# Kernel optimization log

Hardware: AMD Instinct MI355X
Metric: run time of the kernel (lower is better)

Reference implementation:

```python
import jax, jax.numpy as jnp
import numpy as np

B, K, F, INCH, OUTCH, R = 16, 8, 512, 512, 512, 8


def setup_inputs() -> dict:
    key = jax.random.key(0)
    ks = jax.random.split(key, 10)
    inp = {
        "x": jax.random.normal(ks[0], (B, K, F, INCH), jnp.float32),
        "u": jax.random.normal(ks[1], (B, K, OUTCH, R), jnp.float32),
        "v": jax.random.normal(ks[2], (B, K, INCH, R), jnp.float32),
        "b": jax.random.normal(ks[3], (B, 1, 1, OUTCH), jnp.float32) * 0.02,
        # learned parameters (torch nn.Linear layout: W [out, in])
        "W_pass": jax.random.normal(ks[4], (INCH // 2, INCH), jnp.float32) * 0.02,
        "b_pass": jax.random.normal(ks[5], (INCH // 2,), jnp.float32) * 0.02,
        "W_ave": jax.random.normal(ks[6], (INCH // 2, INCH), jnp.float32) * 0.02,
        "b_ave": jax.random.normal(ks[7], (INCH // 2,), jnp.float32) * 0.02,
        "W_out": jax.random.normal(ks[8], (OUTCH, INCH), jnp.float32) * 0.02,
        "b_out": jax.random.normal(ks[9], (OUTCH,), jnp.float32) * 0.02,
    }
    return inp


def reference(x, u, v, b, W_pass, b_pass, W_ave, b_ave, W_out, b_out):
    # x: [B,K,F,inch]
    k = x.shape[1]
    # 'ave' branch: linear -> mean over K -> broadcast back to K
    y = jnp.einsum('bkfi,hi->bkfh', x, W_ave) + b_ave        # [B,K,F,inch//2]
    y = jnp.broadcast_to(jnp.mean(y, axis=1, keepdims=True), y.shape)
    # 'pass' branch
    xp = jnp.einsum('bkfi,hi->bkfh', x, W_pass) + b_pass      # [B,K,F,inch//2]
    h = jnp.concatenate([xp, y], axis=-1)                     # [B,K,F,inch]
    h = jax.nn.gelu(h, approximate=False)                     # dropout is identity in eval
    # LoRA term: mean(v * h) over inch, then mean(u * z) over R
    inch = h.shape[-1]
    r = v.shape[-1]
    z = jnp.einsum('bkfi,bkir->bkfr', h, v) / inch            # [B,K,F,R]
    lora = jnp.einsum('bkfr,bkor->bkfo', z, u) / r            # [B,K,F,outch]
    out = jnp.einsum('bkfi,oi->bkfo', h, W_out) + b_out + lora + b
    out = jax.nn.gelu(out, approximate=False)
    return out
```

## Files before the change

kernel.cpp:

```cpp
#include <hip/hip_runtime.h>
#include <stdint.h>


typedef __attribute__((ext_vector_type(8))) __bf16 bf16x8;
typedef __attribute__((ext_vector_type(4))) float f32x4;
typedef __attribute__((ext_vector_type(8))) unsigned short ushort8;
typedef __attribute__((ext_vector_type(4))) unsigned short ushort4_t;
typedef __attribute__((ext_vector_type(4))) float float4_t;

#define MFMA16(a, b, c) __builtin_amdgcn_mfma_f32_16x16x32_bf16((a), (b), (c), 0, 0, 0)
#define GLL16(g, l)                                                                   \
    __builtin_amdgcn_global_load_lds((const __attribute__((address_space(1))) void*)(g), \
                                     (__attribute__((address_space(3))) void*)(l), 16, 0, 0)

__device__ inline unsigned short f2bf(float f) {
    union { float fv; unsigned u; } un; un.fv = f;
    unsigned u = un.u;
    u += 0x7FFFu + ((u >> 16) & 1u);
    return (unsigned short)(u >> 16);
}

__device__ inline float geluf(float x) {
    float x2 = x * x;
    float inner = x + 0.044715f * x * x2;
    float e = __expf(-1.5957691216057308f * inner);
    return x * __builtin_amdgcn_rcpf(1.0f + e);
}

__device__ inline bf16x8 lds8(const unsigned short* p) {
    return __builtin_bit_cast(bf16x8, *(const ushort8*)p);
}

__device__ inline void stage_chunk(const unsigned short* __restrict__ src, long rowbase,
                                   long stride, int k0, unsigned short* buf, int c, int l) {
    const int r = c * 16 + (l >> 2);
    const int j = (l & 3) ^ ((l >> 2) & 3) ^ (l >> 4);
    GLL16(src + (rowbase + r) * stride + k0 + j * 8, &buf[c * 512]);
}

__device__ inline bf16x8 ldf2(const unsigned short* buf, int rbase, int l) {
    const int r = rbase + (l & 15);
    const int slot = (l >> 4) ^ (r & 3) ^ ((r >> 2) & 3);
    return lds8(&buf[r * 32 + slot * 8]);
}

__device__ inline void stage_w(const unsigned short* __restrict__ src, long rowbase,
                               long stride, int k0, unsigned short* buf, int l) {
#pragma unroll
    for (int it = 0; it < 4; ++it) {
        const int s = it * 64 + l;
        const int r = s >> 2;
        const int j = (s & 3) ^ (r & 3);
        GLL16(src + (rowbase + r) * stride + k0 + j * 8, &buf[it * 512]);
    }
}

__device__ inline bf16x8 ldw(const unsigned short* buf, int rbase, int l) {
    const int r = rbase + (l & 15);
    const int j = l >> 4;
    return lds8(&buf[r * 32 + (((j ^ r) & 3) << 3)]);
}

__global__ void cvt_all(const float* __restrict__ a, const float* __restrict__ b,
                        const float* __restrict__ c, unsigned short* __restrict__ oa,
                        unsigned short* __restrict__ ob, unsigned short* __restrict__ oc) {
    int bid = blockIdx.x;
    const float* s; unsigned short* d; int off;
    if (bid < 128) { s = a; d = oa; off = bid; }
    else if (bid < 256) { s = b; d = ob; off = bid - 128; }
    else { s = c; d = oc; off = bid - 256; }
    int i = off * 256 + threadIdx.x;
    float4_t v = *(const float4_t*)(s + (size_t)i * 4);
    ushort4_t r;
    r[0] = f2bf(v[0]); r[1] = f2bf(v[1]); r[2] = f2bf(v[2]); r[3] = f2bf(v[3]);
    *(ushort4_t*)(d + (size_t)i * 4) = r;
}

__global__ void mean_cvt(const float* __restrict__ x,
                         unsigned short* __restrict__ xb,
                         unsigned short* __restrict__ xm) {
    int gid = blockIdx.x * 256 + threadIdx.x;
    int c  = gid & 63;
    int bf = gid >> 6;
    int b  = bf >> 9;
    int f  = bf & 511;
    float s0 = 0.f, s1 = 0.f, s2 = 0.f, s3 = 0.f, s4 = 0.f, s5 = 0.f, s6 = 0.f, s7 = 0.f;
#pragma unroll
    for (int k = 0; k < 8; ++k) {
        long row = (long)(b * 8 + k) * 512 + f;
        float4_t lo = *(const float4_t*)(x + row * 512 + c * 8);
        float4_t hi = *(const float4_t*)(x + row * 512 + c * 8 + 4);
        s0 += lo[0]; s1 += lo[1]; s2 += lo[2]; s3 += lo[3];
        s4 += hi[0]; s5 += hi[1]; s6 += hi[2]; s7 += hi[3];
        ushort8 t;
        t[0] = f2bf(lo[0]); t[1] = f2bf(lo[1]); t[2] = f2bf(lo[2]); t[3] = f2bf(lo[3]);
        t[4] = f2bf(hi[0]); t[5] = f2bf(hi[1]); t[6] = f2bf(hi[2]); t[7] = f2bf(hi[3]);
        *(ushort8*)(xb + row * 512 + c * 8) = t;
    }
    ushort8 m;
    m[0] = f2bf(s0 * 0.125f); m[1] = f2bf(s1 * 0.125f);
    m[2] = f2bf(s2 * 0.125f); m[3] = f2bf(s3 * 0.125f);
    m[4] = f2bf(s4 * 0.125f); m[5] = f2bf(s5 * 0.125f);
    m[6] = f2bf(s6 * 0.125f); m[7] = f2bf(s7 * 0.125f);
    *(ushort8*)(xm + (long)bf * 512 + c * 8) = m;
}

__launch_bounds__(256)
__global__ void gemm_gelu(const unsigned short* __restrict__ A,
                          const unsigned short* __restrict__ W,
                          const float* __restrict__ bias,
                          unsigned short* __restrict__ O,
                          int chunk) {
    __shared__ __align__(16) unsigned short S[32768];
    const int tid = threadIdx.x;
    const int w = tid >> 6, l = tid & 63;
    const int wr = w >> 1, wc = w & 1;
    const int work = ((blockIdx.x & 7) * chunk) + (blockIdx.x >> 3);
    const int nt = work & 1;
    const int mt = work >> 1;
    const long row0 = (long)mt * 128 + wr * 64;
    const long col0 = (long)nt * 128 + wc * 64;

    unsigned short* aw[2] = { &S[w * 4096],        &S[16384 + w * 4096] };
    unsigned short* bw[2] = { &S[w * 4096 + 2048], &S[16384 + w * 4096 + 2048] };

    f32x4 acc[4][4];
    const f32x4 z4 = {0.f, 0.f, 0.f, 0.f};
#pragma unroll
    for (int i = 0; i < 4; ++i)
#pragma unroll
        for (int j = 0; j < 4; ++j) acc[i][j] = z4;

    stage_w(A, row0, 512, 0, aw[0], l);
    stage_w(W, col0, 512, 0, bw[0], l);

#pragma unroll
    for (int t = 0; t < 16; ++t) {
        if (t < 15) {
            stage_w(A, row0, 512, (t + 1) * 32, aw[(t + 1) & 1], l);
            stage_w(W, col0, 512, (t + 1) * 32, bw[(t + 1) & 1], l);
            asm volatile("s_waitcnt vmcnt(8)" ::: "memory");
        } else {
            asm volatile("s_waitcnt vmcnt(0)" ::: "memory");
        }
        const unsigned short* ab = aw[t & 1];
        const unsigned short* bbuf = bw[t & 1];
        bf16x8 af[4], bfr[4];
#pragma unroll
        for (int mi = 0; mi < 4; ++mi) af[mi] = ldw(ab, mi * 16, l);
#pragma unroll
        for (int nj = 0; nj < 4; ++nj) bfr[nj] = ldw(bbuf, nj * 16, l);
        __builtin_amdgcn_s_setprio(1);
#pragma unroll
        for (int mi = 0; mi < 4; ++mi)
#pragma unroll
            for (int nj = 0; nj < 4; ++nj)
                acc[mi][nj] = MFMA16(af[mi], bfr[nj], acc[mi][nj]);
        __builtin_amdgcn_s_setprio(0);
    }

    __syncthreads();
    const int colblk = nt * 128;
#pragma unroll
    for (int mi = 0; mi < 4; ++mi) {
        const int R0 = wr * 64 + mi * 16 + (l >> 4) * 4;
#pragma unroll
        for (int nj = 0; nj < 4; ++nj) {
            const int C = wc * 64 + nj * 16 + (l & 15);
            const float bv = bias[colblk + C];
#pragma unroll
            for (int q = 0; q < 4; ++q)
                S[(R0 + q) * 136 + C] = f2bf(geluf(acc[mi][nj][q] + bv));
        }
    }
    __syncthreads();
    const long rowt = (long)mt * 128;
#pragma unroll
    for (int s = 0; s < 8; ++s) {
        const int flat = s * 2048 + tid * 8;
        const int row = flat >> 7;
        const int col = flat & 127;
        ushort8 vv = *(const ushort8*)&S[row * 136 + col];
        *(ushort8*)(O + (rowt + row) * 256 + colblk + col) = vv;
    }
}

__launch_bounds__(256)
__global__ void g2calc(const unsigned short* __restrict__ Gy,
                       const unsigned short* __restrict__ Wo,
                       const float* __restrict__ bo,
                       float* __restrict__ G2) {
    __shared__ __align__(16) unsigned short S[32768];
    const int tid = threadIdx.x;
    const int w = tid >> 6, l = tid & 63;
    const int wr = w >> 1, wc = w & 1;
    const int mt = blockIdx.x >> 2;
    const int nt = blockIdx.x & 3;
    const long row0 = (long)mt * 128 + wr * 64;
    const long col0 = (long)nt * 128 + wc * 64;

    unsigned short* aw[2] = { &S[w * 4096],        &S[16384 + w * 4096] };
    unsigned short* bw[2] = { &S[w * 4096 + 2048], &S[16384 + w * 4096 + 2048] };

    f32x4 acc[4][4];
    const f32x4 z4 = {0.f, 0.f, 0.f, 0.f};
#pragma unroll
    for (int i = 0; i < 4; ++i)
#pragma unroll
        for (int j = 0; j < 4; ++j) acc[i][j] = z4;

    stage_w(Gy, row0, 256, 0, aw[0], l);
    stage_w(Wo, col0, 512, 256, bw[0], l);

#pragma unroll
    for (int t = 0; t < 8; ++t) {
        if (t < 7) {
            stage_w(Gy, row0, 256, (t + 1) * 32, aw[(t + 1) & 1], l);
            stage_w(Wo, col0, 512, 256 + (t + 1) * 32, bw[(t + 1) & 1], l);
            asm volatile("s_waitcnt vmcnt(8)" ::: "memory");
        } else {
            asm volatile("s_waitcnt vmcnt(0)" ::: "memory");
        }
        const unsigned short* ab = aw[t & 1];
        const unsigned short* bbuf = bw[t & 1];
        bf16x8 af[4], bfr[4];
#pragma unroll
        for (int mi = 0; mi < 4; ++mi) af[mi] = ldw(ab, mi * 16, l);
#pragma unroll
        for (int nj = 0; nj < 4; ++nj) bfr[nj] = ldw(bbuf, nj * 16, l);
#pragma unroll
        for (int mi = 0; mi < 4; ++mi)
#pragma unroll
            for (int nj = 0; nj < 4; ++nj)
                acc[mi][nj] = MFMA16(af[mi], bfr[nj], acc[mi][nj]);
    }

#pragma unroll
    for (int mi = 0; mi < 4; ++mi) {
        const long rb = row0 + mi * 16 + (l >> 4) * 4;
#pragma unroll
        for (int nj = 0; nj < 4; ++nj) {
            const long cg = col0 + nj * 16 + (l & 15);
            const float bv = bo[cg];
#pragma unroll
            for (int q = 0; q < 4; ++q)
                G2[(rb + q) * 512 + cg] = acc[mi][nj][q] + bv;
        }
    }
}

__launch_bounds__(512)
__global__ void fused_out(const unsigned short* __restrict__ xb,
                          const unsigned short* __restrict__ Wp,
                          const float* __restrict__ bp,
                          const unsigned short* __restrict__ Gy,
                          const unsigned short* __restrict__ Wo,
                          const float* __restrict__ bbi,
                          const float* __restrict__ u,
                          const float* __restrict__ v,
                          const float* __restrict__ G2,
                          float* __restrict__ Out) {
    __shared__ __align__(16) unsigned short hp_t[128 * 256];
    __shared__ __align__(16) unsigned short stg[2 * 12288];
    __shared__ __align__(16) unsigned short Vt[16 * 536];
    __shared__ __align__(16) unsigned short Zs[128 * 32];

    const int tid = threadIdx.x;
    const int w = tid >> 6, l = tid & 63;
    const int wm = w >> 2, wn = w & 3;
    const int mt = ((blockIdx.x & 7) * 64) + (blockIdx.x >> 3);
    const long row0 = (long)mt * 128;
    const int bk = mt >> 2;
    const int bi = bk >> 3;
    const int f0 = (mt & 3) * 128;
    const long gyb = (long)bi * 512 + f0;

    const f32x4 zero4 = {0.f, 0.f, 0.f, 0.f};

    {
        f32x4 acc[4][4];
#pragma unroll
        for (int i = 0; i < 4; ++i)
#pragma unroll
            for (int j = 0; j < 4; ++j) acc[i][j] = zero4;

#define STAGE1(t)                                                             \
    {                                                                         \
        const int kb = (t) * 32;                                              \
        unsigned short* bA = &stg[((t) & 1) * 12288];                         \
        unsigned short* bB = bA + 4096;                                       \
        stage_chunk(xb, row0, 512, kb, bA, w, l);                             \
        stage_chunk(Wp, 0, 512, kb, bB, 2 * w, l);                            \
        stage_chunk(Wp, 0, 512, kb, bB, 2 * w + 1, l);                        \
    }

        STAGE1(0)
#pragma unroll
        for (int t = 0; t < 16; ++t) {
            __builtin_amdgcn_s_barrier();
            if (t < 15) {
                STAGE1(t + 1)
                asm volatile("s_waitcnt vmcnt(3)" ::: "memory");
            } else {
                asm volatile("s_waitcnt vmcnt(0)" ::: "memory");
            }
            const unsigned short* bA = &stg[(t & 1) * 12288];
            const unsigned short* bB = bA + 4096;
            bf16x8 a[4], b[4];
#pragma unroll
            for (int mi = 0; mi < 4; ++mi) a[mi] = ldf2(bA, wm * 64 + mi * 16, l);
#pragma unroll
            for (int nj = 0; nj < 4; ++nj) b[nj] = ldf2(bB, wn * 64 + nj * 16, l);
            __builtin_amdgcn_s_setprio(1);
#pragma unroll
            for (int mi = 0; mi < 4; ++mi)
#pragma unroll
                for (int nj = 0; nj < 4; ++nj)
                    acc[mi][nj] = MFMA16(a[mi], b[nj], acc[mi][nj]);
            __builtin_amdgcn_s_setprio(0);
        }
#undef STAGE1

#pragma unroll
        for (int mi = 0; mi < 4; ++mi) {
            const int R0 = wm * 64 + mi * 16 + (l >> 4) * 4;
#pragma unroll
            for (int nj = 0; nj < 4; ++nj) {
                const int C = wn * 64 + nj * 16 + (l & 15);
                const float bv = bp[C];
#pragma unroll
                for (int q = 0; q < 4; ++q) {
                    const int row = R0 + q;
                    const int slot = (C >> 3) ^ (row & 31);
                    hp_t[row * 256 + slot * 8 + (C & 7)] =
                        f2bf(geluf(acc[mi][nj][q] + bv));
                }
            }
        }
        ushort8 zz = {0, 0, 0, 0, 0, 0, 0, 0};
        *(ushort8*)&Zs[tid * 8] = zz;
        for (int i = tid; i < 1072; i += 512) *(ushort8*)&Vt[i * 8] = zz;
    }
    __syncthreads();

#define STAGE2(t)                                                              \
    {                                                                          \
        const int ch = (t) >> 3;                                               \
        const int kb = ((t) & 7) * 32;                                         \
        unsigned short* bB = &stg[((t) & 1) * 12288];                          \
        stage_chunk(Wo, (long)ch * 256, 512, kb, bB, 2 * w, l);                \
        stage_chunk(Wo, (long)ch * 256, 512, kb, bB, 2 * w + 1, l);            \
    }
    STAGE2(0)
    {
        const float* vp = v + (long)bk * 4096;
        float4_t v0 = *(const float4_t*)(vp + tid * 8);
        float4_t v1 = *(const float4_t*)(vp + tid * 8 + 4);
#pragma unroll
        for (int j = 0; j < 8; ++j) {
            const int flat = tid * 8 + j;
            const float val = (j < 4 ? v0[j] : v1[j - 4]) * (1.0f / 512.0f);
            Vt[(flat & 7) * 536 + (flat >> 3)] = f2bf(val);
        }
    }
    __syncthreads();

    {
        f32x4 zacc = zero4;
        const int zrow = w * 16 + (l & 15);
#pragma unroll
        for (int ks = 0; ks < 8; ++ks) {
            const int jw = ks * 4 + (l >> 4);
            bf16x8 av = lds8(&hp_t[zrow * 256 + ((jw ^ (zrow & 31)) * 8)]);
            bf16x8 bv = lds8(&Vt[(l & 15) * 536 + ks * 32 + (l >> 4) * 8]);
            zacc = MFMA16(av, bv, zacc);
        }
        const unsigned short* grow = Gy + (gyb + zrow) * 256 + (l >> 4) * 8;
#pragma unroll
        for (int ks = 0; ks < 8; ++ks) {
            bf16x8 bv = lds8(&Vt[(l & 15) * 536 + 256 + ks * 32 + (l >> 4) * 8]);
            zacc = MFMA16(lds8(grow + ks * 32), bv, zacc);
        }
        if ((l & 15) < 8) {
#pragma unroll
            for (int reg = 0; reg < 4; ++reg)
                Zs[(w * 16 + (l >> 4) * 4 + reg) * 32 + (l & 15)] = f2bf(zacc[reg]);
        }
    }

    f32x4 acc2[2][4][4];
#pragma unroll
    for (int c = 0; c < 2; ++c)
#pragma unroll
        for (int i = 0; i < 4; ++i)
#pragma unroll
            for (int j = 0; j < 4; ++j) acc2[c][i][j] = zero4;

#pragma unroll
    for (int t = 0; t < 16; ++t) {
        __builtin_amdgcn_s_barrier();
        if (t < 15) {
            STAGE2(t + 1)
            asm volatile("s_waitcnt vmcnt(2)" ::: "memory");
        } else {
            asm volatile("s_waitcnt vmcnt(0)" ::: "memory");
        }
        const unsigned short* bB = &stg[(t & 1) * 12288];
        bf16x8 a[4], b[4];
#pragma unroll
        for (int mi = 0; mi < 4; ++mi) {
            const int row = wm * 64 + mi * 16 + (l & 15);
            const int jw = (t & 7) * 4 + (l >> 4);
            a[mi] = lds8(&hp_t[row * 256 + ((jw ^ (row & 31)) * 8)]);
        }
#pragma unroll
        for (int nj = 0; nj < 4; ++nj) b[nj] = ldf2(bB, wn * 64 + nj * 16, l);
        __builtin_amdgcn_s_setprio(1);
#pragma unroll
        for (int mi = 0; mi < 4; ++mi)
#pragma unroll
            for (int nj = 0; nj < 4; ++nj)
                acc2[t >> 3][mi][nj] = MFMA16(a[mi], b[nj], acc2[t >> 3][mi][nj]);
        __builtin_amdgcn_s_setprio(0);
    }
#undef STAGE2

    const float* up = u + (long)bk * 4096;
#pragma unroll
    for (int ch = 0; ch < 2; ++ch) {
#pragma unroll
        for (int nj = 0; nj < 4; ++nj) {
            const int og = ch * 256 + wn * 64 + nj * 16 + (l & 15);
            ushort8 ubits = {0, 0, 0, 0, 0, 0, 0, 0};
            if ((l >> 4) == 0) {
                float4_t u0 = *(const float4_t*)(up + og * 8);
                float4_t u1 = *(const float4_t*)(up + og * 8 + 4);
                ubits[0] = f2bf(u0[0] * 0.125f); ubits[1] = f2bf(u0[1] * 0.125f);
                ubits[2] = f2bf(u0[2] * 0.125f); ubits[3] = f2bf(u0[3] * 0.125f);
                ubits[4] = f2bf(u1[0] * 0.125f); ubits[5] = f2bf(u1[1] * 0.125f);
                ubits[6] = f2bf(u1[2] * 0.125f); ubits[7] = f2bf(u1[3] * 0.125f);
            }
            bf16x8 ub = __builtin_bit_cast(bf16x8, ubits);
#pragma unroll
            for (int mi = 0; mi < 4; ++mi) {
                bf16x8 az = lds8(&Zs[(wm * 64 + mi * 16 + (l & 15)) * 32 + (l >> 4) * 8]);
                acc2[ch][mi][nj] = MFMA16(az, ub, acc2[ch][mi][nj]);
            }
        }
    }

#pragma unroll
    for (int ch = 0; ch < 2; ++ch) {
#pragma unroll
        for (int nj = 0; nj < 4; ++nj) {
            const int og = ch * 256 + wn * 64 + nj * 16 + (l & 15);
            const float badd = bbi[bi * 512 + og];
#pragma unroll
            for (int mi = 0; mi < 4; ++mi) {
                const int R0 = wm * 64 + mi * 16 + (l >> 4) * 4;
#pragma unroll
                for (int q = 0; q < 4; ++q) {
                    const float g2v = G2[(gyb + R0 + q) * 512 + og];
                    __builtin_nontemporal_store(
                        geluf(acc2[ch][mi][nj][q] + badd + g2v),
                        Out + (row0 + R0 + q) * 512 + og);
                }
            }
        }
    }
}

extern "C" void kernel_launch(void* const* d_in, const int* in_sizes, int n_in,
                              void* d_out, int out_size, void* d_ws, size_t ws_size,
                              hipStream_t stream) {
    const float* x  = (const float*)d_in[0];
    const float* u  = (const float*)d_in[1];
    const float* v  = (const float*)d_in[2];
    const float* bb = (const float*)d_in[3];
    const float* Wp = (const float*)d_in[4];
    const float* bp = (const float*)d_in[5];
    const float* Wa = (const float*)d_in[6];
    const float* ba = (const float*)d_in[7];
    const float* Wo = (const float*)d_in[8];
    const float* bo = (const float*)d_in[9];
    float* out = (float*)d_out;

    char* ws = (char*)d_ws;
    unsigned short* xb  = (unsigned short*)(ws + 0);
    unsigned short* xm  = (unsigned short*)(ws + 67108864);
    unsigned short* gy  = (unsigned short*)(ws + 75497472);
    float*          G2  = (float*)(ws + 79691776);
    unsigned short* Wpb = (unsigned short*)(ws + 96468992);
    unsigned short* Wab = (unsigned short*)(ws + 96731136);
    unsigned short* Wob = (unsigned short*)(ws + 96993280);

    cvt_all<<<512, 256, 0, stream>>>(Wp, Wa, Wo, Wpb, Wab, Wob);
    mean_cvt<<<2048, 256, 0, stream>>>(x, xb, xm);
    gemm_gelu<<<128, 256, 0, stream>>>(xm, Wab, ba, gy, 16);
    g2calc<<<256, 256, 0, stream>>>(gy, Wob, bo, G2);
    fused_out<<<512, 512, 0, stream>>>(xb, Wpb, bp, gy, Wob, bb, u, v, G2, out);
}
```

Before: 148.1 us.

## Halve fused_out row tile to 64 and restructure pipelines for higher occupancy

The fused output kernel now processes 64-row tiles instead of 128, with 1024 blocks, smaller LDS buffers and accumulator arrays, and launch bounds asking for 4 blocks per CU. The pass-GEMM is split into two 128-column chunks written to hp_t at chunk ends, the output GEMM runs over four 128-column chunks, and the LoRA MFMA is merged into the epilogue. The goal is to cut register and LDS pressure so more waves hide latency. The cost is that each block reloads the full weight matrices for half as many rows, so weight traffic per output row doubles, and the loops add extra barriers.

Result: slower. 154.9 us (+4.6%).

```diff
diff --git a/kernel.cpp b/kernel.cpp
--- a/kernel.cpp
+++ b/kernel.cpp
@@ -249,7 +249,7 @@
     }
 }
 
-__launch_bounds__(512)
+__launch_bounds__(512, 4)
 __global__ void fused_out(const unsigned short* __restrict__ xb,
                           const unsigned short* __restrict__ Wp,
                           const float* __restrict__ bp,
@@ -260,99 +260,98 @@
                           const float* __restrict__ v,
                           const float* __restrict__ G2,
                           float* __restrict__ Out) {
-    __shared__ __align__(16) unsigned short hp_t[128 * 256];
-    __shared__ __align__(16) unsigned short stg[2 * 12288];
-    __shared__ __align__(16) unsigned short Vt[16 * 536];
-    __shared__ __align__(16) unsigned short Zs[128 * 32];
+    __shared__ __align__(16) unsigned short hp_t[64 * 256];
+    __shared__ __align__(16) unsigned short stg[2 * 6144];
+    __shared__ __align__(16) unsigned short Vt[16 * 520];
+    __shared__ __align__(16) unsigned short Zs[64 * 32];
 
     const int tid = threadIdx.x;
     const int w = tid >> 6, l = tid & 63;
     const int wm = w >> 2, wn = w & 3;
-    const int mt = ((blockIdx.x & 7) * 64) + (blockIdx.x >> 3);
-    const long row0 = (long)mt * 128;
-    const int bk = mt >> 2;
+    const int mt = ((blockIdx.x & 7) * 128) + (blockIdx.x >> 3);
+    const long row0 = (long)mt * 64;
+    const int bk = mt >> 3;
     const int bi = bk >> 3;
-    const int f0 = (mt & 3) * 128;
-    const long gyb = (long)bi * 512 + f0;
+    const long gyb = (long)bi * 512 + (mt & 7) * 64;
 
     const f32x4 zero4 = {0.f, 0.f, 0.f, 0.f};
 
     {
-        f32x4 acc[4][4];
-#pragma unroll
-        for (int i = 0; i < 4; ++i)
-#pragma unroll
-            for (int j = 0; j < 4; ++j) acc[i][j] = zero4;
-
-#define STAGE1(t)                                                             \
+        f32x4 acc[2][2];
+#pragma unroll
+        for (int i = 0; i < 2; ++i)
+#pragma unroll
+            for (int j = 0; j < 2; ++j) acc[i][j] = zero4;
+
+#define STG1(s)                                                               \
     {                                                                         \
-        const int kb = (t) * 32;                                              \
-        unsigned short* bA = &stg[((t) & 1) * 12288];                         \
-        unsigned short* bB = bA + 4096;                                       \
-        stage_chunk(xb, row0, 512, kb, bA, w, l);                             \
-        stage_chunk(Wp, 0, 512, kb, bB, 2 * w, l);                            \
-        stage_chunk(Wp, 0, 512, kb, bB, 2 * w + 1, l);                        \
-    }
-
-        STAGE1(0)
-#pragma unroll
-        for (int t = 0; t < 16; ++t) {
-            __builtin_amdgcn_s_barrier();
-            if (t < 15) {
-                STAGE1(t + 1)
-                asm volatile("s_waitcnt vmcnt(3)" ::: "memory");
+        const int ch_ = (s) >> 4, kb_ = ((s) & 15) * 32;                      \
+        unsigned short* base_ = &stg[((s) & 1) * 6144];                       \
+        stage_chunk(Wp, (long)ch_ * 128, 512, kb_, base_ + 2048, w, l);       \
+        if (w < 4) stage_chunk(xb, row0, 512, kb_, base_, w, l);              \
+    }
+
+        STG1(0)
+#pragma unroll
+        for (int s = 0; s < 32; ++s) {
+            if (s < 31) {
+                STG1(s + 1)
+                if (w < 4) asm volatile("s_waitcnt vmcnt(2)" ::: "memory");
+                else       asm volatile("s_waitcnt vmcnt(1)" ::: "memory");
             } else {
                 asm volatile("s_waitcnt vmcnt(0)" ::: "memory");
             }
-            const unsigned short* bA = &stg[(t & 1) * 12288];
-            const unsigned short* bB = bA + 4096;
-            bf16x8 a[4], b[4];
-#pragma unroll
-            for (int mi = 0; mi < 4; ++mi) a[mi] = ldf2(bA, wm * 64 + mi * 16, l);
-#pragma unroll
-            for (int nj = 0; nj < 4; ++nj) b[nj] = ldf2(bB, wn * 64 + nj * 16, l);
+            __builtin_amdgcn_s_barrier();
+            const unsigned short* bufA = &stg[(s & 1) * 6144];
+            const unsigned short* bufB = bufA + 2048;
+            bf16x8 a[2], b[2];
+#pragma unroll
+            for (int mi = 0; mi < 2; ++mi) a[mi] = ldf2(bufA, wm * 32 + mi * 16, l);
+#pragma unroll
+            for (int nj = 0; nj < 2; ++nj) b[nj] = ldf2(bufB, wn * 32 + nj * 16, l);
             __builtin_amdgcn_s_setprio(1);
 #pragma unroll
-            for (int mi = 0; mi < 4; ++mi)
-#pragma unroll
-                for (int nj = 0; nj < 4; ++nj)
+            for (int mi = 0; mi < 2; ++mi)
+#pragma unroll
+                for (int nj = 0; nj < 2; ++nj)
                     acc[mi][nj] = MFMA16(a[mi], b[nj], acc[mi][nj]);
             __builtin_amdgcn_s_setprio(0);
-        }
-#undef STAGE1
-
-#pragma unroll
-        for (int mi = 0; mi < 4; ++mi) {
-            const int R0 = wm * 64 + mi * 16 + (l >> 4) * 4;
-#pragma unroll
-            for (int nj = 0; nj < 4; ++nj) {
-                const int C = wn * 64 + nj * 16 + (l & 15);
-                const float bv = bp[C];
-#pragma unroll
-                for (int q = 0; q < 4; ++q) {
-                    const int row = R0 + q;
-                    const int slot = (C >> 3) ^ (row & 31);
-                    hp_t[row * 256 + slot * 8 + (C & 7)] =
-                        f2bf(geluf(acc[mi][nj][q] + bv));
+            if (s == 15 || s == 31) {
+                const int ch = s >> 4;
+#pragma unroll
+                for (int mi = 0; mi < 2; ++mi) {
+#pragma unroll
+                    for (int nj = 0; nj < 2; ++nj) {
+                        const int C = ch * 128 + wn * 32 + nj * 16 + (l & 15);
+                        const float bv = bp[C];
+#pragma unroll
+                        for (int q = 0; q < 4; ++q) {
+                            const int row = wm * 32 + mi * 16 + (l >> 4) * 4 + q;
+                            const int slot = (C >> 3) ^ (row & 31);
+                            hp_t[row * 256 + slot * 8 + (C & 7)] =
+                                f2bf(geluf(acc[mi][nj][q] + bv));
+                        }
+                        acc[mi][nj] = zero4;
+                    }
                 }
+                asm volatile("s_waitcnt lgkmcnt(0)" ::: "memory");
             }
-        }
+            __builtin_amdgcn_s_barrier();
+        }
+#undef STG1
+    }
+
+#define STG2(s)                                                               \
+    {                                                                         \
+        const int ch_ = (s) >> 3, kb_ = ((s) & 7) * 32;                       \
+        stage_chunk(Wo, (long)ch_ * 128, 512, kb_, &stg[((s) & 1) * 6144], w, l); \
+    }
+    {
+        ushort4_t z4s = {0, 0, 0, 0};
+        *(ushort4_t*)&Zs[tid * 4] = z4s;
         ushort8 zz = {0, 0, 0, 0, 0, 0, 0, 0};
-        *(ushort8*)&Zs[tid * 8] = zz;
-        for (int i = tid; i < 1072; i += 512) *(ushort8*)&Vt[i * 8] = zz;
-    }
-    __syncthreads();
-
-#define STAGE2(t)                                                              \
-    {                                                                          \
-        const int ch = (t) >> 3;                                               \
-        const int kb = ((t) & 7) * 32;                                         \
-        unsigned short* bB = &stg[((t) & 1) * 12288];                          \
-        stage_chunk(Wo, (long)ch * 256, 512, kb, bB, 2 * w, l);                \
-        stage_chunk(Wo, (long)ch * 256, 512, kb, bB, 2 * w + 1, l);            \
-    }
-    STAGE2(0)
-    {
+        for (int i = tid; i < 520; i += 512)
+            *(ushort8*)&Vt[4160 + i * 8] = zz;
         const float* vp = v + (long)bk * 4096;
         float4_t v0 = *(const float4_t*)(vp + tid * 8);
         float4_t v1 = *(const float4_t*)(vp + tid * 8 + 4);
@@ -360,25 +359,27 @@
         for (int j = 0; j < 8; ++j) {
             const int flat = tid * 8 + j;
             const float val = (j < 4 ? v0[j] : v1[j - 4]) * (1.0f / 512.0f);
-            Vt[(flat & 7) * 536 + (flat >> 3)] = f2bf(val);
-        }
-    }
-    __syncthreads();
-
-    {
+            Vt[(flat & 7) * 520 + (flat >> 3)] = f2bf(val);
+        }
+        STG2(0)
+        asm volatile("s_waitcnt lgkmcnt(0)" ::: "memory");
+        __builtin_amdgcn_s_barrier();
+    }
+
+    if (w < 4) {
         f32x4 zacc = zero4;
         const int zrow = w * 16 + (l & 15);
 #pragma unroll
         for (int ks = 0; ks < 8; ++ks) {
             const int jw = ks * 4 + (l >> 4);
             bf16x8 av = lds8(&hp_t[zrow * 256 + ((jw ^ (zrow & 31)) * 8)]);
-            bf16x8 bv = lds8(&Vt[(l & 15) * 536 + ks * 32 + (l >> 4) * 8]);
+            bf16x8 bv = lds8(&Vt[(l & 15) * 520 + ks * 32 + (l >> 4) * 8]);
             zacc = MFMA16(av, bv, zacc);
         }
         const unsigned short* grow = Gy + (gyb + zrow) * 256 + (l >> 4) * 8;
 #pragma unroll
         for (int ks = 0; ks < 8; ++ks) {
-            bf16x8 bv = lds8(&Vt[(l & 15) * 536 + 256 + ks * 32 + (l >> 4) * 8]);
+            bf16x8 bv = lds8(&Vt[(l & 15) * 520 + 256 + ks * 32 + (l >> 4) * 8]);
             zacc = MFMA16(lds8(grow + ks * 32), bv, zacc);
         }
         if ((l & 15) < 8) {
@@ -386,51 +387,53 @@
             for (int reg = 0; reg < 4; ++reg)
                 Zs[(w * 16 + (l >> 4) * 4 + reg) * 32 + (l & 15)] = f2bf(zacc[reg]);
         }
-    }
-
-    f32x4 acc2[2][4][4];
-#pragma unroll
-    for (int c = 0; c < 2; ++c)
-#pragma unroll
-        for (int i = 0; i < 4; ++i)
-#pragma unroll
-            for (int j = 0; j < 4; ++j) acc2[c][i][j] = zero4;
-
-#pragma unroll
-    for (int t = 0; t < 16; ++t) {
-        __builtin_amdgcn_s_barrier();
-        if (t < 15) {
-            STAGE2(t + 1)
-            asm volatile("s_waitcnt vmcnt(2)" ::: "memory");
+        asm volatile("s_waitcnt lgkmcnt(0)" ::: "memory");
+    }
+
+    f32x4 acc2[4][2][2];
+#pragma unroll
+    for (int c = 0; c < 4; ++c)
+#pragma unroll
+        for (int i = 0; i < 2; ++i)
+#pragma unroll
+            for (int j = 0; j < 2; ++j) acc2[c][i][j] = zero4;
+
+#pragma unroll
+    for (int s = 0; s < 32; ++s) {
+        if (s < 31) {
+            STG2(s + 1)
+            asm volatile("s_waitcnt vmcnt(1)" ::: "memory");
         } else {
             asm volatile("s_waitcnt vmcnt(0)" ::: "memory");
         }
-        const unsigned short* bB = &stg[(t & 1) * 12288];
-        bf16x8 a[4], b[4];
-#pragma unroll
-        for (int mi = 0; mi < 4; ++mi) {
-            const int row = wm * 64 + mi * 16 + (l & 15);
-            const int jw = (t & 7) * 4 + (l >> 4);
+        __builtin_amdgcn_s_barrier();
+        const unsigned short* bufB = &stg[(s & 1) * 6144];
+        bf16x8 a[2], b[2];
+#pragma unroll
+        for (int mi = 0; mi < 2; ++mi) {
+            const int row = wm * 32 + mi * 16 + (l & 15);
+            const int jw = (s & 7) * 4 + (l >> 4);
             a[mi] = lds8(&hp_t[row * 256 + ((jw ^ (row & 31)) * 8)]);
         }
 #pragma unroll
-        for (int nj = 0; nj < 4; ++nj) b[nj] = ldf2(bB, wn * 64 + nj * 16, l);
+        for (int nj = 0; nj < 2; ++nj) b[nj] = ldf2(bufB, wn * 32 + nj * 16, l);
         __builtin_amdgcn_s_setprio(1);
 #pragma unroll
-        for (int mi = 0; mi < 4; ++mi)
-#pragma unroll
-            for (int nj = 0; nj < 4; ++nj)
-                acc2[t >> 3][mi][nj] = MFMA16(a[mi], b[nj], acc2[t >> 3][mi][nj]);
+        for (int mi = 0; mi < 2; ++mi)
+#pragma unroll
+            for (int nj = 0; nj < 2; ++nj)
+                acc2[s >> 3][mi][nj] = MFMA16(a[mi], b[nj], acc2[s >> 3][mi][nj]);
         __builtin_amdgcn_s_setprio(0);
-    }
-#undef STAGE2
+        __builtin_amdgcn_s_barrier();
+    }
+#undef STG2
 
     const float* up = u + (long)bk * 4096;
 #pragma unroll
-    for (int ch = 0; ch < 2; ++ch) {
-#pragma unroll
-        for (int nj = 0; nj < 4; ++nj) {
-            const int og = ch * 256 + wn * 64 + nj * 16 + (l & 15);
+    for (int ch = 0; ch < 4; ++ch) {
+#pragma unroll
+        for (int nj = 0; nj < 2; ++nj) {
+            const int og = ch * 128 + wn * 32 + nj * 16 + (l & 15);
             ushort8 ubits = {0, 0, 0, 0, 0, 0, 0, 0};
             if ((l >> 4) == 0) {
                 float4_t u0 = *(const float4_t*)(up + og * 8);
@@ -441,29 +444,18 @@
                 ubits[6] = f2bf(u1[2] * 0.125f); ubits[7] = f2bf(u1[3] * 0.125f);
             }
             bf16x8 ub = __builtin_bit_cast(bf16x8, ubits);
-#pragma unroll
-            for (int mi = 0; mi < 4; ++mi) {
-                bf16x8 az = lds8(&Zs[(wm * 64 + mi * 16 + (l & 15)) * 32 + (l >> 4) * 8]);
-                acc2[ch][mi][nj] = MFMA16(az, ub, acc2[ch][mi][nj]);
-            }
-        }
-    }
-
-#pragma unroll
-    for (int ch = 0; ch < 2; ++ch) {
-#pragma unroll
-        for (int nj = 0; nj < 4; ++nj) {
-            const int og = ch * 256 + wn * 64 + nj * 16 + (l & 15);
             const float badd = bbi[bi * 512 + og];
 #pragma unroll
-            for (int mi = 0; mi < 4; ++mi) {
-                const int R0 = wm * 64 + mi * 16 + (l >> 4) * 4;
+            for (int mi = 0; mi < 2; ++mi) {
+                bf16x8 az = lds8(&Zs[(wm * 32 + mi * 16 + (l & 15)) * 32 + (l >> 4) * 8]);
+                f32x4 r = MFMA16(az, ub, acc2[ch][mi][nj]);
 #pragma unroll
                 for (int q = 0; q < 4; ++q) {
-                    const float g2v = G2[(gyb + R0 + q) * 512 + og];
+                    const int row = wm * 32 + mi * 16 + (l >> 4) * 4 + q;
+                    const float g2v = G2[(gyb + row) * 512 + og];
                     __builtin_nontemporal_store(
-                        geluf(acc2[ch][mi][nj][q] + badd + g2v),
-                        Out + (row0 + R0 + q) * 512 + og);
+                        geluf(r[q] + badd + g2v),
+                        Out + (row0 + row) * 512 + og);
                 }
             }
         }
@@ -498,5 +490,5 @@
     mean_cvt<<<2048, 256, 0, stream>>>(x, xb, xm);
     gemm_gelu<<<128, 256, 0, stream>>>(xm, Wab, ba, gy, 16);
     g2calc<<<256, 256, 0, stream>>>(gy, Wob, bo, G2);
-    fused_out<<<512, 512, 0, stream>>>(xb, Wpb, bp, gy, Wob, bb, u, v, G2, out);
-}
+    fused_out<<<1024, 512, 0, stream>>>(xb, Wpb, bp, gy, Wob, bb, u, v, G2, out);
+}
```

## Double k-step depth per stage and alias phase-1 staging into hp_t LDS

Applied to the files above, without the earlier changes.

Both GEMM phases in fused_out now stage 64-wide K slices per iteration instead of 32, halving the number of barrier-separated steps and issuing twice as many MFMAs per step. The shared memory is merged into one buffer so phase-1 double buffering reuses the hp_t region (free until GELU output is written), which provides room for the larger stages. Barriers move to after the wait and after compute to guard buffer reuse. This may raise LDS footprint and register pressure and changes wait-count bookkeeping, which could hurt occupancy or correctness if the counts are off.

Measured after the change: 141.8 us. -4.2%, faster.

```diff
diff --git a/kernel.cpp b/kernel.cpp
--- a/kernel.cpp
+++ b/kernel.cpp
@@ -260,10 +260,11 @@
                           const float* __restrict__ v,
                           const float* __restrict__ G2,
                           float* __restrict__ Out) {
-    __shared__ __align__(16) unsigned short hp_t[128 * 256];
-    __shared__ __align__(16) unsigned short stg[2 * 12288];
-    __shared__ __align__(16) unsigned short Vt[16 * 536];
-    __shared__ __align__(16) unsigned short Zs[128 * 32];
+    __shared__ __align__(16) unsigned short SM[78208];
+    unsigned short* hp_t = &SM[0];
+    unsigned short* Sreg = &SM[32768];
+    unsigned short* Vt   = &SM[65536];
+    unsigned short* Zs   = &SM[74112];
 
     const int tid = threadIdx.x;
     const int w = tid >> 6, l = tid & 63;
@@ -277,6 +278,17 @@
 
     const f32x4 zero4 = {0.f, 0.f, 0.f, 0.f};
 
+#define STG1(t)                                                               \
+    {                                                                         \
+        unsigned short* b_ = ((t) & 1) ? hp_t : Sreg;                         \
+        const int kb_ = (t) * 64;                                             \
+        stage_chunk(xb, row0, 512, kb_,      b_,         w, l);               \
+        stage_chunk(xb, row0, 512, kb_ + 32, b_ + 4096,  w, l);               \
+        stage_chunk(Wp, 0,    512, kb_,      b_ + 8192,  2 * w,     l);       \
+        stage_chunk(Wp, 0,    512, kb_,      b_ + 8192,  2 * w + 1, l);       \
+        stage_chunk(Wp, 0,    512, kb_ + 32, b_ + 16384, 2 * w,     l);       \
+        stage_chunk(Wp, 0,    512, kb_ + 32, b_ + 16384, 2 * w + 1, l);       \
+    }
     {
         f32x4 acc[4][4];
 #pragma unroll
@@ -284,42 +296,39 @@
 #pragma unroll
             for (int j = 0; j < 4; ++j) acc[i][j] = zero4;
 
-#define STAGE1(t)                                                             \
-    {                                                                         \
-        const int kb = (t) * 32;                                              \
-        unsigned short* bA = &stg[((t) & 1) * 12288];                         \
-        unsigned short* bB = bA + 4096;                                       \
-        stage_chunk(xb, row0, 512, kb, bA, w, l);                             \
-        stage_chunk(Wp, 0, 512, kb, bB, 2 * w, l);                            \
-        stage_chunk(Wp, 0, 512, kb, bB, 2 * w + 1, l);                        \
-    }
-
-        STAGE1(0)
-#pragma unroll
-        for (int t = 0; t < 16; ++t) {
-            __builtin_amdgcn_s_barrier();
-            if (t < 15) {
-                STAGE1(t + 1)
-                asm volatile("s_waitcnt vmcnt(3)" ::: "memory");
+        STG1(0)
+#pragma unroll
+        for (int t = 0; t < 8; ++t) {
+            if (t < 7) {
+                STG1(t + 1)
+                asm volatile("s_waitcnt vmcnt(6)" ::: "memory");
             } else {
                 asm volatile("s_waitcnt vmcnt(0)" ::: "memory");
             }
-            const unsigned short* bA = &stg[(t & 1) * 12288];
-            const unsigned short* bB = bA + 4096;
-            bf16x8 a[4], b[4];
-#pragma unroll
-            for (int mi = 0; mi < 4; ++mi) a[mi] = ldf2(bA, wm * 64 + mi * 16, l);
-#pragma unroll
-            for (int nj = 0; nj < 4; ++nj) b[nj] = ldf2(bB, wn * 64 + nj * 16, l);
+            __builtin_amdgcn_s_barrier();
+            const unsigned short* b_ = (t & 1) ? hp_t : Sreg;
+            bf16x8 a[4][2], b[4][2];
+#pragma unroll
+            for (int mi = 0; mi < 4; ++mi) {
+                a[mi][0] = ldf2(b_,        wm * 64 + mi * 16, l);
+                a[mi][1] = ldf2(b_ + 4096, wm * 64 + mi * 16, l);
+            }
+#pragma unroll
+            for (int nj = 0; nj < 4; ++nj) {
+                b[nj][0] = ldf2(b_ + 8192,  wn * 64 + nj * 16, l);
+                b[nj][1] = ldf2(b_ + 16384, wn * 64 + nj * 16, l);
+            }
             __builtin_amdgcn_s_setprio(1);
 #pragma unroll
             for (int mi = 0; mi < 4; ++mi)
 #pragma unroll
-                for (int nj = 0; nj < 4; ++nj)
-                    acc[mi][nj] = MFMA16(a[mi], b[nj], acc[mi][nj]);
+                for (int nj = 0; nj < 4; ++nj) {
+                    acc[mi][nj] = MFMA16(a[mi][0], b[nj][0], acc[mi][nj]);
+                    acc[mi][nj] = MFMA16(a[mi][1], b[nj][1], acc[mi][nj]);
+                }
             __builtin_amdgcn_s_setprio(0);
-        }
-#undef STAGE1
+            __builtin_amdgcn_s_barrier();
+        }
 
 #pragma unroll
         for (int mi = 0; mi < 4; ++mi) {
@@ -341,18 +350,20 @@
         *(ushort8*)&Zs[tid * 8] = zz;
         for (int i = tid; i < 1072; i += 512) *(ushort8*)&Vt[i * 8] = zz;
     }
+#undef STG1
     __syncthreads();
 
-#define STAGE2(t)                                                              \
-    {                                                                          \
-        const int ch = (t) >> 3;                                               \
-        const int kb = ((t) & 7) * 32;                                         \
-        unsigned short* bB = &stg[((t) & 1) * 12288];                          \
-        stage_chunk(Wo, (long)ch * 256, 512, kb, bB, 2 * w, l);                \
-        stage_chunk(Wo, (long)ch * 256, 512, kb, bB, 2 * w + 1, l);            \
-    }
-    STAGE2(0)
+#define STG2(s)                                                               \
+    {                                                                         \
+        const int ch_ = (s) >> 2, kk_ = ((s) & 3) * 64;                       \
+        unsigned short* b_ = Sreg + ((s) & 1) * 16384;                        \
+        stage_chunk(Wo, (long)ch_ * 256, 512, kk_,      b_,        2 * w,     l); \
+        stage_chunk(Wo, (long)ch_ * 256, 512, kk_,      b_,        2 * w + 1, l); \
+        stage_chunk(Wo, (long)ch_ * 256, 512, kk_ + 32, b_ + 8192, 2 * w,     l); \
+        stage_chunk(Wo, (long)ch_ * 256, 512, kk_ + 32, b_ + 8192, 2 * w + 1, l); \
+    }
     {
+        STG2(0)
         const float* vp = v + (long)bk * 4096;
         float4_t v0 = *(const float4_t*)(vp + tid * 8);
         float4_t v1 = *(const float4_t*)(vp + tid * 8 + 4);
@@ -362,6 +373,7 @@
             const float val = (j < 4 ? v0[j] : v1[j - 4]) * (1.0f / 512.0f);
             Vt[(flat & 7) * 536 + (flat >> 3)] = f2bf(val);
         }
+        asm volatile("s_waitcnt vmcnt(0)" ::: "memory");
     }
     __syncthreads();
 
@@ -386,6 +398,7 @@
             for (int reg = 0; reg < 4; ++reg)
                 Zs[(w * 16 + (l >> 4) * 4 + reg) * 32 + (l & 15)] = f2bf(zacc[reg]);
         }
+        asm volatile("s_waitcnt lgkmcnt(0)" ::: "memory");
     }
 
     f32x4 acc2[2][4][4];
@@ -397,33 +410,46 @@
             for (int j = 0; j < 4; ++j) acc2[c][i][j] = zero4;
 
 #pragma unroll
-    for (int t = 0; t < 16; ++t) {
-        __builtin_amdgcn_s_barrier();
-        if (t < 15) {
-            STAGE2(t + 1)
-            asm volatile("s_waitcnt vmcnt(2)" ::: "memory");
-        } else {
-            asm volatile("s_waitcnt vmcnt(0)" ::: "memory");
-        }
-        const unsigned short* bB = &stg[(t & 1) * 12288];
-        bf16x8 a[4], b[4];
-#pragma unroll
-        for (int mi = 0; mi < 4; ++mi) {
-            const int row = wm * 64 + mi * 16 + (l & 15);
-            const int jw = (t & 7) * 4 + (l >> 4);
-            a[mi] = lds8(&hp_t[row * 256 + ((jw ^ (row & 31)) * 8)]);
-        }
-#pragma unroll
-        for (int nj = 0; nj < 4; ++nj) b[nj] = ldf2(bB, wn * 64 + nj * 16, l);
-        __builtin_amdgcn_s_setprio(1);
-#pragma unroll
-        for (int mi = 0; mi < 4; ++mi)
-#pragma unroll
-            for (int nj = 0; nj < 4; ++nj)
-                acc2[t >> 3][mi][nj] = MFMA16(a[mi], b[nj], acc2[t >> 3][mi][nj]);
-        __builtin_amdgcn_s_setprio(0);
-    }
-#undef STAGE2
+    for (int ch = 0; ch < 2; ++ch) {
+#pragma unroll
+        for (int kk = 0; kk < 4; ++kk) {
+            const int s = ch * 4 + kk;
+            if (s < 7) {
+                STG2(s + 1)
+                asm volatile("s_waitcnt vmcnt(4)" ::: "memory");
+            } else {
+                asm volatile("s_waitcnt vmcnt(0)" ::: "memory");
+            }
+            __builtin_amdgcn_s_barrier();
+            const unsigned short* b_ = Sreg + (s & 1) * 16384;
+            bf16x8 a[4][2], b[4][2];
+#pragma unroll
+            for (int mi = 0; mi < 4; ++mi) {
+                const int row = wm * 64 + mi * 16 + (l & 15);
+#pragma unroll
+                for (int ks = 0; ks < 2; ++ks) {
+                    const int jw = kk * 8 + ks * 4 + (l >> 4);
+                    a[mi][ks] = lds8(&hp_t[row * 256 + ((jw ^ (row & 31)) * 8)]);
+                }
+            }
+#pragma unroll
+            for (int nj = 0; nj < 4; ++nj) {
+                b[nj][0] = ldf2(b_,        wn * 64 + nj * 16, l);
+                b[nj][1] = ldf2(b_ + 8192, wn * 64 + nj * 16, l);
+            }
+            __builtin_amdgcn_s_setprio(1);
+#pragma unroll
+            for (int mi = 0; mi < 4; ++mi)
+#pragma unroll
+                for (int nj = 0; nj < 4; ++nj) {
+                    acc2[ch][mi][nj] = MFMA16(a[mi][0], b[nj][0], acc2[ch][mi][nj]);
+                    acc2[ch][mi][nj] = MFMA16(a[mi][1], b[nj][1], acc2[ch][mi][nj]);
+                }
+            __builtin_amdgcn_s_setprio(0);
+            __builtin_amdgcn_s_barrier();
+        }
+    }
+#undef STG2
 
     const float* up = u + (long)bk * 4096;
 #pragma unroll
```
